# Kernel optimization log

Hardware: AMD Instinct MI355X
Metric: run time of the kernel (lower is better)

## Reference

```python
import jax, jax.numpy as jnp
import numpy as np

N, IN_DIM, OUT_DIM = 8192, 128, 64
ALPHA = 0.2  # LeakyReLU negative slope
NEG_INF = -1e12


def setup_inputs() -> dict:
    key = jax.random.key(0)
    k1, k2, k3, k4 = jax.random.split(key, 4)
    x = jax.random.normal(k1, (N, IN_DIM), dtype=jnp.float32)
    adj = jax.random.randint(k2, (N, N), 0, 2, dtype=jnp.int32)
    W = jax.random.normal(k3, (IN_DIM, OUT_DIM), dtype=jnp.float32) * 0.1
    a = jax.random.normal(k4, (2 * OUT_DIM, 1), dtype=jnp.float32) * 0.1
    return {"x": x, "adj": adj, "W": W, "a": a}


def reference(x, adj, W, a):
    Wh = x @ W                                   # [N, out_dim]
    Wh1 = Wh @ a[:OUT_DIM, :]                    # [N, 1] source scores
    Wh2 = Wh @ a[OUT_DIM:, :]                    # [N, 1] target scores
    e = Wh1 + Wh2.T                              # [N, N] additive attention
    e = jnp.where(e > 0, e, ALPHA * e)           # LeakyReLU
    scores = jnp.where(adj > 0, e, NEG_INF)      # mask non-edges
    attention = jax.nn.softmax(scores, axis=1)   # row-wise softmax
    h_prime = attention @ Wh                     # [N, out_dim]
    return jax.nn.elu(h_prime)
```

## Files before the change

kernel.cpp:

```cpp
#include <hip/hip_runtime.h>


#define N 8192
#define IN_DIM 128
#define OUT_DIM 64
#define ALPHA 0.2f
#define JC 8
#define JTILES (N / JC / 64)

typedef _Float16 half8 __attribute__((ext_vector_type(8)));
typedef float f32x4 __attribute__((ext_vector_type(4)));

__global__ __launch_bounds__(64) void wh_kernel(
    const float* __restrict__ x, const float* __restrict__ W,
    const float* __restrict__ a, _Float16* __restrict__ Wh_t,
    float* __restrict__ s1, float* __restrict__ s2) {
  __shared__ float xs[IN_DIM];
  const int i = blockIdx.x;
  const int t = threadIdx.x;

  xs[t]      = x[(size_t)i * IN_DIM + t];
  xs[t + 64] = x[(size_t)i * IN_DIM + 64 + t];
  __syncthreads();

  float wh = 0.f;
#pragma unroll
  for (int d = 0; d < IN_DIM; ++d) wh = fmaf(xs[d], W[d * OUT_DIM + t], wh);

  Wh_t[(size_t)t * N + i] = (_Float16)wh;

  float p1 = wh * a[t];
  float p2 = wh * a[64 + t];
#pragma unroll
  for (int off = 32; off; off >>= 1) {
    p1 += __shfl_down(p1, off);
    p2 += __shfl_down(p2, off);
  }
  if (t == 0) {
    s1[i] = p1;
    s2[i] = p2;
  }
}

__global__ __launch_bounds__(256) void max_kernel(
    const float* __restrict__ s1, const float* __restrict__ s2,
    float* __restrict__ Mout) {
  __shared__ float red[8];
  const int t = threadIdx.x;
  float m1 = -1e30f, m2 = -1e30f;
  for (int idx = t; idx < N; idx += 256) {
    m1 = fmaxf(m1, s1[idx]);
    m2 = fmaxf(m2, s2[idx]);
  }
#pragma unroll
  for (int off = 32; off; off >>= 1) {
    m1 = fmaxf(m1, __shfl_down(m1, off));
    m2 = fmaxf(m2, __shfl_down(m2, off));
  }
  if ((t & 63) == 0) {
    red[t >> 6] = m1;
    red[4 + (t >> 6)] = m2;
  }
  __syncthreads();
  if (t == 0) {
    m1 = fmaxf(fmaxf(red[0], red[1]), fmaxf(red[2], red[3]));
    m2 = fmaxf(fmaxf(red[4], red[5]), fmaxf(red[6], red[7]));
    float e = m1 + m2;
    Mout[0] = e > 0.f ? e : ALPHA * e;
  }
}

__global__ __launch_bounds__(256, 4) void attn_kernel(
    const int* __restrict__ adj, const _Float16* __restrict__ Wh_t,
    const float* __restrict__ s1, const float* __restrict__ s2,
    const float* __restrict__ Mptr, float* __restrict__ accp,
    float* __restrict__ lp) {
  const int t = threadIdx.x;
  const int w = t >> 6;
  const int lane = t & 63;
  const int q = lane >> 4;
  const int r16 = lane & 15;
  const int i0 = blockIdx.x * 64 + w * 16;
  const int c = blockIdx.y;
  const int jbase = c * (N / JC);

  const float M = Mptr[0];
  const float s1v = s1[i0 + r16];
  const size_t arow = (size_t)(i0 + r16) * N;

  f32x4 acc[4] = {{0.f, 0.f, 0.f, 0.f},
                  {0.f, 0.f, 0.f, 0.f},
                  {0.f, 0.f, 0.f, 0.f},
                  {0.f, 0.f, 0.f, 0.f}};
  float lacc = 0.f;

  for (int jt = 0; jt < JTILES; ++jt) {
    const int j0 = jbase + jt * 64;

    half8 aF[2];
#pragma unroll
    for (int ks = 0; ks < 2; ++ks) {
      const int kb = ks * 32 + q * 8;
      const int4 a0 = *(const int4*)(adj + arow + j0 + kb);
      const int4 a1 = *(const int4*)(adj + arow + j0 + kb + 4);
      const float4 sa = *(const float4*)(s2 + j0 + kb);
      const float4 sb = *(const float4*)(s2 + j0 + kb + 4);
      const int av[8] = {a0.x, a0.y, a0.z, a0.w, a1.x, a1.y, a1.z, a1.w};
      const float sv[8] = {sa.x, sa.y, sa.z, sa.w, sb.x, sb.y, sb.z, sb.w};
#pragma unroll
      for (int cc = 0; cc < 8; ++cc) {
        float e = s1v + sv[cc];
        e = e > 0.f ? e : ALPHA * e;
        float pv = __expf(e - M);
        pv = av[cc] > 0 ? pv : 0.f;
        _Float16 h = (_Float16)pv;
        aF[ks][cc] = h;
        lacc += (float)h;
      }
    }

#pragma unroll
    for (int ks = 0; ks < 2; ++ks) {
      const int kb = ks * 32 + q * 8;
#pragma unroll
      for (int fg = 0; fg < 4; ++fg) {
        const half8 bf =
            *(const half8*)(Wh_t + (size_t)(fg * 16 + r16) * N + j0 + kb);
        acc[fg] = __builtin_amdgcn_mfma_f32_16x16x32_f16(aF[ks], bf, acc[fg],
                                                         0, 0, 0);
      }
    }
  }

  lacc += __shfl_xor(lacc, 16);
  lacc += __shfl_xor(lacc, 32);
  if (q == 0) lp[(size_t)c * N + i0 + r16] = lacc;

#pragma unroll
  for (int fg = 0; fg < 4; ++fg) {
#pragma unroll
    for (int r = 0; r < 4; ++r) {
      const int row = i0 + q * 4 + r;
      accp[((size_t)c * N + row) * OUT_DIM + fg * 16 + r16] = acc[fg][r];
    }
  }
}

__global__ __launch_bounds__(256) void reduce_kernel(
    const float* __restrict__ accp, const float* __restrict__ lp,
    float* __restrict__ out) {
  const int tid = blockIdx.x * 256 + threadIdx.x;
  const int i = tid >> 6;
  float s = 0.f, l = 0.f;
#pragma unroll
  for (int c = 0; c < JC; ++c) s += accp[(size_t)c * N * OUT_DIM + tid];
#pragma unroll
  for (int c = 0; c < JC; ++c) l += lp[(size_t)c * N + i];
  float v = s / l;
  out[tid] = v > 0.f ? v : expm1f(v);
}

extern "C" void kernel_launch(void* const* d_in, const int* in_sizes, int n_in,
                              void* d_out, int out_size, void* d_ws,
                              size_t ws_size, hipStream_t stream) {
  const float* x = (const float*)d_in[0];
  const int* adj = (const int*)d_in[1];
  const float* W = (const float*)d_in[2];
  const float* a = (const float*)d_in[3];
  float* out = (float*)d_out;

  char* ws = (char*)d_ws;
  _Float16* Wh_t = (_Float16*)ws;
  float* s1 = (float*)(ws + (size_t)N * OUT_DIM * 2);
  float* s2 = s1 + N;
  float* M = s2 + N;
  float* accp = (float*)(ws + (2u << 20));
  float* lp = accp + (size_t)JC * N * OUT_DIM;

  wh_kernel<<<N, 64, 0, stream>>>(x, W, a, Wh_t, s1, s2);
  max_kernel<<<1, 256, 0, stream>>>(s1, s2, M);
  attn_kernel<<<dim3(N / 64, JC), 256, 0, stream>>>(adj, Wh_t, s1, s2, M,
                                                    accp, lp);
  reduce_kernel<<<N * OUT_DIM / 256, 256, 0, stream>>>(accp, lp, out);
}
```

Before: 442.7 us.

## Coalesce adjacency loads via LDS-staged P tile and MFMA row sums

Reworks the attention kernel so each half-wave reads 128 contiguous adjacency ints per row, instead of 16 rows of short strided segments. The masked exp values are written to a per-wave LDS tile and reloaded as MFMA A-fragments. The softmax denominator is now computed by an extra MFMA against a ones vector, replacing the scalar accumulation and shuffles. Exponentials use exp2 with log2e pre-folded into the scores, and the column split and occupancy hint are doubled. The cost is an LDS round trip, one extra MFMA per k-step, and larger partial buffers for the reduce kernel.

After: 449.3 us. Within noise of the previous version (+1.5%).

```diff
diff --git a/kernel.cpp b/kernel.cpp
--- a/kernel.cpp
+++ b/kernel.cpp
@@ -5,16 +5,22 @@
 #define IN_DIM 128
 #define OUT_DIM 64
 #define ALPHA 0.2f
-#define JC 8
-#define JTILES (N / JC / 64)
+#define LOG2E 1.44269504088896f
+#define JC 16
+#define CW (N / JC)
+#define TW 128
+#define NT (CW / TW)
+#define LDP 136
 
 typedef _Float16 half8 __attribute__((ext_vector_type(8)));
+typedef _Float16 half4 __attribute__((ext_vector_type(4)));
 typedef float f32x4 __attribute__((ext_vector_type(4)));
 
 __global__ __launch_bounds__(64) void wh_kernel(
     const float* __restrict__ x, const float* __restrict__ W,
     const float* __restrict__ a, _Float16* __restrict__ Wh_t,
-    float* __restrict__ s1, float* __restrict__ s2) {
+    float* __restrict__ s1, float* __restrict__ s2,
+    float* __restrict__ s2L) {
   __shared__ float xs[IN_DIM];
   const int i = blockIdx.x;
   const int t = threadIdx.x;
@@ -39,6 +45,7 @@
   if (t == 0) {
     s1[i] = p1;
     s2[i] = p2;
+    s2L[i] = p2 * LOG2E;
   }
 }
 
@@ -70,79 +77,93 @@
   }
 }
 
-__global__ __launch_bounds__(256, 4) void attn_kernel(
+__global__ __launch_bounds__(256, 8) void attn_kernel(
     const int* __restrict__ adj, const _Float16* __restrict__ Wh_t,
-    const float* __restrict__ s1, const float* __restrict__ s2,
+    const float* __restrict__ s1, const float* __restrict__ s2L,
     const float* __restrict__ Mptr, float* __restrict__ accp,
     float* __restrict__ lp) {
+  __shared__ __align__(16) _Float16 Ps[4 * 16 * LDP];
+
   const int t = threadIdx.x;
   const int w = t >> 6;
   const int lane = t & 63;
   const int q = lane >> 4;
   const int r16 = lane & 15;
+  const int half_ = lane >> 5;
+  const int l32 = lane & 31;
   const int i0 = blockIdx.x * 64 + w * 16;
   const int c = blockIdx.y;
-  const int jbase = c * (N / JC);
-
-  const float M = Mptr[0];
-  const float s1v = s1[i0 + r16];
-  const size_t arow = (size_t)(i0 + r16) * N;
-
-  f32x4 acc[4] = {{0.f, 0.f, 0.f, 0.f},
-                  {0.f, 0.f, 0.f, 0.f},
-                  {0.f, 0.f, 0.f, 0.f},
+  const int jb = c * CW;
+
+  const float ML = Mptr[0] * LOG2E;
+
+  float s1L[8];
+#pragma unroll
+  for (int it = 0; it < 8; ++it)
+    s1L[it] = s1[i0 + 2 * it + half_] * LOG2E;
+
+  half8 bones;
+#pragma unroll
+  for (int e = 0; e < 8; ++e) bones[e] = (r16 == 0) ? (_Float16)1.0f : (_Float16)0.0f;
+
+  f32x4 acc[5] = {{0.f, 0.f, 0.f, 0.f}, {0.f, 0.f, 0.f, 0.f},
+                  {0.f, 0.f, 0.f, 0.f}, {0.f, 0.f, 0.f, 0.f},
                   {0.f, 0.f, 0.f, 0.f}};
-  float lacc = 0.f;
-
-  for (int jt = 0; jt < JTILES; ++jt) {
-    const int j0 = jbase + jt * 64;
-
-    half8 aF[2];
-#pragma unroll
-    for (int ks = 0; ks < 2; ++ks) {
-      const int kb = ks * 32 + q * 8;
-      const int4 a0 = *(const int4*)(adj + arow + j0 + kb);
-      const int4 a1 = *(const int4*)(adj + arow + j0 + kb + 4);
-      const float4 sa = *(const float4*)(s2 + j0 + kb);
-      const float4 sb = *(const float4*)(s2 + j0 + kb + 4);
-      const int av[8] = {a0.x, a0.y, a0.z, a0.w, a1.x, a1.y, a1.z, a1.w};
-      const float sv[8] = {sa.x, sa.y, sa.z, sa.w, sb.x, sb.y, sb.z, sb.w};
-#pragma unroll
-      for (int cc = 0; cc < 8; ++cc) {
-        float e = s1v + sv[cc];
-        e = e > 0.f ? e : ALPHA * e;
-        float pv = __expf(e - M);
-        pv = av[cc] > 0 ? pv : 0.f;
-        _Float16 h = (_Float16)pv;
-        aF[ks][cc] = h;
-        lacc += (float)h;
-      }
+
+  _Float16* Pw = Ps + w * 16 * LDP;
+  const _Float16* ldA = Pw + r16 * LDP + q * 8;
+  _Float16* stP = Pw + half_ * LDP + l32 * 4;
+
+  for (int jt = 0; jt < NT; ++jt) {
+    const int j0 = jb + jt * TW;
+
+    const float4 sv = *(const float4*)(s2L + j0 + l32 * 4);
+    const int* ap = adj + (size_t)(i0 + half_) * N + j0 + l32 * 4;
+
+#pragma unroll
+    for (int it = 0; it < 8; ++it) {
+      const int4 av = *(const int4*)(ap + (size_t)it * (2 * N));
+      const float s1v = s1L[it];
+      float p0, p1, p2, p3, tt, uu;
+      tt = s1v + sv.x; uu = fmaxf(tt, ALPHA * tt); p0 = exp2f(uu - ML);
+      tt = s1v + sv.y; uu = fmaxf(tt, ALPHA * tt); p1 = exp2f(uu - ML);
+      tt = s1v + sv.z; uu = fmaxf(tt, ALPHA * tt); p2 = exp2f(uu - ML);
+      tt = s1v + sv.w; uu = fmaxf(tt, ALPHA * tt); p3 = exp2f(uu - ML);
+      half4 hv;
+      hv[0] = (_Float16)(av.x != 0 ? p0 : 0.f);
+      hv[1] = (_Float16)(av.y != 0 ? p1 : 0.f);
+      hv[2] = (_Float16)(av.z != 0 ? p2 : 0.f);
+      hv[3] = (_Float16)(av.w != 0 ? p3 : 0.f);
+      *(half4*)(stP + it * (2 * LDP)) = hv;
     }
 
 #pragma unroll
-    for (int ks = 0; ks < 2; ++ks) {
-      const int kb = ks * 32 + q * 8;
+    for (int ks = 0; ks < 4; ++ks) {
+      const half8 aF = *(const half8*)(ldA + ks * 32);
+      const int kcol = j0 + ks * 32 + q * 8;
 #pragma unroll
       for (int fg = 0; fg < 4; ++fg) {
         const half8 bf =
-            *(const half8*)(Wh_t + (size_t)(fg * 16 + r16) * N + j0 + kb);
-        acc[fg] = __builtin_amdgcn_mfma_f32_16x16x32_f16(aF[ks], bf, acc[fg],
-                                                         0, 0, 0);
+            *(const half8*)(Wh_t + (size_t)(fg * 16 + r16) * N + kcol);
+        acc[fg] =
+            __builtin_amdgcn_mfma_f32_16x16x32_f16(aF, bf, acc[fg], 0, 0, 0);
       }
+      acc[4] =
+          __builtin_amdgcn_mfma_f32_16x16x32_f16(aF, bones, acc[4], 0, 0, 0);
     }
   }
 
-  lacc += __shfl_xor(lacc, 16);
-  lacc += __shfl_xor(lacc, 32);
-  if (q == 0) lp[(size_t)c * N + i0 + r16] = lacc;
-
 #pragma unroll
   for (int fg = 0; fg < 4; ++fg) {
 #pragma unroll
     for (int r = 0; r < 4; ++r) {
-      const int row = i0 + q * 4 + r;
-      accp[((size_t)c * N + row) * OUT_DIM + fg * 16 + r16] = acc[fg][r];
+      accp[((size_t)c * N + i0 + q * 4 + r) * OUT_DIM + fg * 16 + r16] =
+          acc[fg][r];
     }
+  }
+  if (r16 == 0) {
+#pragma unroll
+    for (int r = 0; r < 4; ++r) lp[(size_t)c * N + i0 + q * 4 + r] = acc[4][r];
   }
 }
 
@@ -171,15 +192,16 @@
 
   char* ws = (char*)d_ws;
   _Float16* Wh_t = (_Float16*)ws;
-  float* s1 = (float*)(ws + (size_t)N * OUT_DIM * 2);
+  float* s1 = (float*)(ws + (1u << 20));
   float* s2 = s1 + N;
-  float* M = s2 + N;
+  float* s2L = s2 + N;
+  float* M = s2L + N;
   float* accp = (float*)(ws + (2u << 20));
   float* lp = accp + (size_t)JC * N * OUT_DIM;
 
-  wh_kernel<<<N, 64, 0, stream>>>(x, W, a, Wh_t, s1, s2);
+  wh_kernel<<<N, 64, 0, stream>>>(x, W, a, Wh_t, s1, s2, s2L);
   max_kernel<<<1, 256, 0, stream>>>(s1, s2, M);
-  attn_kernel<<<dim3(N / 64, JC), 256, 0, stream>>>(adj, Wh_t, s1, s2, M,
+  attn_kernel<<<dim3(N / 64, JC), 256, 0, stream>>>(adj, Wh_t, s1, s2L, M,
                                                     accp, lp);
   reduce_kernel<<<N * OUT_DIM / 256, 256, 0, stream>>>(accp, lp, out);
 }
```
